# Kernel optimization log

Measured on AMD Instinct MI355X. Metric: run time of the kernel, lower is better.

## Reference

```python
import jax, jax.numpy as jnp
import numpy as np

S = 7
STEP = 1.0 / S
LAMBDA_COORD = 5.0
LAMBDA_NOOBJ = 0.5


def setup_inputs() -> dict:
    key = jax.random.key(0)
    k1, k2, k3 = jax.random.split(key, 3)
    B = 16384
    pred = jax.random.uniform(k1, (B, S, S, 30), dtype=jnp.float32)
    target = jax.random.uniform(k2, (B, S, S, 30), dtype=jnp.float32)
    conf = (jax.random.uniform(k3, (B, S, S)) > 0.9).astype(jnp.float32)
    target = target.at[..., 4].set(conf)
    return {"pred": pred, "target": target}


def _convert_box(box):
    # box: [..., S, S, 4] in cell-relative (x, y, w, h); returns clipped corners.
    gi = jnp.arange(S, dtype=box.dtype).reshape(1, S, 1)  # first spatial axis -> x offset
    gj = jnp.arange(S, dtype=box.dtype).reshape(1, 1, S)  # second spatial axis -> y offset
    x, y, w, h = box[..., 0], box[..., 1], box[..., 2], box[..., 3]
    cx = (x + gi) * STEP
    cy = (y + gj) * STEP
    x1 = jnp.maximum(cx - w / 2, 0.0)
    y1 = jnp.maximum(cy - h / 2, 0.0)
    x2 = jnp.minimum(cx + w / 2, 1.0)
    y2 = jnp.minimum(cy + h / 2, 1.0)
    return x1, y1, x2, y2


def _iou(b1, b2):
    a, b, c, d = b1
    q, w, e, r = b2
    minx = jnp.maximum(a, q)
    miny = jnp.maximum(b, w)
    maxx = jnp.minimum(c, e)
    maxy = jnp.minimum(d, r)
    inter = (maxy - miny) * (maxx - minx)  # faithful: no clamping of negative overlaps
    union = (e - q) * (r - w) + (d - b) * (c - a) - inter
    return jnp.where(inter > 0, inter / (union + 1e-05), 0.0)


def reference(pred, target):
    B = pred.shape[0]
    tbox = _convert_box(target[..., :4])
    pbox1 = _convert_box(pred[..., 0:4])
    pbox2 = _convert_box(pred[..., 5:9])
    iou1 = _iou(tbox, pbox1)  # [B, S, S]
    iou2 = _iou(tbox, pbox2)

    sel2 = iou1 <= iou2  # original: box1 responsible only if iou1 > iou2
    conf_t = jax.lax.stop_gradient(jnp.where(sel2, iou2, iou1))  # .item() detached iou
    pxy = jnp.where(sel2[..., None], pred[..., 5:7], pred[..., 0:2])
    pwh = jnp.where(sel2[..., None], pred[..., 7:9], pred[..., 2:4])
    pconf = jnp.where(sel2, pred[..., 9], pred[..., 4])

    obj = (target[..., 4] > 0).astype(pred.dtype)  # [B, S, S]
    noobj = (target[..., 4] == 0).astype(pred.dtype)

    obj_loss = jnp.sum(obj * (pconf - conf_t) ** 2)
    xy_loss = jnp.sum(obj[..., None] * (pxy - target[..., 0:2]) ** 2)
    wh_loss = jnp.sum(obj[..., None] * (pwh - target[..., 2:4]) ** 2)
    class_loss = jnp.sum(obj[..., None] * (pred[..., 10:] - target[..., 10:]) ** 2)
    noobj_loss = jnp.sum(noobj * ((pred[..., 4] - target[..., 4]) ** 2 + (pred[..., 9] - target[..., 9]) ** 2))

    loss = obj_loss + LAMBDA_NOOBJ * noobj_loss + LAMBDA_COORD * (xy_loss + wh_loss) + class_loss
    return loss / B
```

## Files before the change

### kernel.cpp

```cpp
#include <hip/hip_runtime.h>


#define NS 7
#define NC 30
#define CPB 128
#define BLOCK 128
#define CHUNK_FLOATS (CPB * NC)
#define GRID1 6272

typedef __attribute__((address_space(1))) const float global_float;
typedef __attribute__((address_space(3))) float lds_float;

__global__ __launch_bounds__(BLOCK) void yolo_loss_stage1(
    const float* __restrict__ pred,
    const float* __restrict__ targ,
    float* __restrict__ partials)
{
    const float STEP = 1.0f / 7.0f;
    const float L_COORD = 5.0f;
    const float L_NOOBJ = 0.5f;

    __shared__ float sbuf[2 * CHUNK_FLOATS];

    const int tid = threadIdx.x;
    const int wave = tid >> 6;
    const int lane = tid & 63;

    {
        const size_t base_bytes = (size_t)blockIdx.x * (CHUNK_FLOATS * 4);
        const char* gbase = (const char*)(wave == 0 ? pred : targ) + base_bytes
                          + (size_t)lane * 16;
        char* lbase = (char*)sbuf + wave * (CHUNK_FLOATS * 4);
        #pragma unroll
        for (int i = 0; i < 15; ++i) {
            __builtin_amdgcn_global_load_lds(
                (global_float*)(gbase + i * 1024),
                (lds_float*)(lbase + i * 1024),
                16, 0, 0);
        }
    }
    __syncthreads();

    const int cell = blockIdx.x * CPB + tid;
    const int j = cell % NS;
    const int i = (cell / NS) % NS;
    const float gi = (float)i;
    const float gj = (float)j;

    float p[NC], t[NC];
    {
        const float2* lp2 = (const float2*)(sbuf + tid * NC);
        const float2* lt2 = (const float2*)(sbuf + CHUNK_FLOATS + tid * NC);
        #pragma unroll
        for (int k = 0; k < NC / 2; ++k) {
            float2 v = lp2[k]; p[2 * k] = v.x; p[2 * k + 1] = v.y;
            float2 u = lt2[k]; t[2 * k] = u.x; t[2 * k + 1] = u.y;
        }
    }

    float ta, tb, tc, td;
    {
        float cx = (t[0] + gi) * STEP;
        float cy = (t[1] + gj) * STEP;
        ta = fmaxf(cx - t[2] * 0.5f, 0.0f);
        tb = fmaxf(cy - t[3] * 0.5f, 0.0f);
        tc = fminf(cx + t[2] * 0.5f, 1.0f);
        td = fminf(cy + t[3] * 0.5f, 1.0f);
    }
    float q1, w1, e1, r1;
    {
        float cx = (p[0] + gi) * STEP;
        float cy = (p[1] + gj) * STEP;
        q1 = fmaxf(cx - p[2] * 0.5f, 0.0f);
        w1 = fmaxf(cy - p[3] * 0.5f, 0.0f);
        e1 = fminf(cx + p[2] * 0.5f, 1.0f);
        r1 = fminf(cy + p[3] * 0.5f, 1.0f);
    }
    float q2, w2, e2, r2;
    {
        float cx = (p[5] + gi) * STEP;
        float cy = (p[6] + gj) * STEP;
        q2 = fmaxf(cx - p[7] * 0.5f, 0.0f);
        w2 = fmaxf(cy - p[8] * 0.5f, 0.0f);
        e2 = fminf(cx + p[7] * 0.5f, 1.0f);
        r2 = fminf(cy + p[8] * 0.5f, 1.0f);
    }

    float tarea = (td - tb) * (tc - ta);
    float iou1, iou2;
    {
        float minx = fmaxf(ta, q1), miny = fmaxf(tb, w1);
        float maxx = fminf(tc, e1), maxy = fminf(td, r1);
        float inter = (maxy - miny) * (maxx - minx);
        float uni = (e1 - q1) * (r1 - w1) + tarea - inter;
        iou1 = (inter > 0.0f) ? inter / (uni + 1e-5f) : 0.0f;
    }
    {
        float minx = fmaxf(ta, q2), miny = fmaxf(tb, w2);
        float maxx = fminf(tc, e2), maxy = fminf(td, r2);
        float inter = (maxy - miny) * (maxx - minx);
        float uni = (e2 - q2) * (r2 - w2) + tarea - inter;
        iou2 = (inter > 0.0f) ? inter / (uni + 1e-5f) : 0.0f;
    }

    bool sel2 = (iou1 <= iou2);
    float conf_t = sel2 ? iou2 : iou1;
    float px = sel2 ? p[5] : p[0];
    float py = sel2 ? p[6] : p[1];
    float pw = sel2 ? p[7] : p[2];
    float ph = sel2 ? p[8] : p[3];
    float pconf = sel2 ? p[9] : p[4];

    float obj = (t[4] > 0.0f) ? 1.0f : 0.0f;
    float noobj = (t[4] == 0.0f) ? 1.0f : 0.0f;

    float dx = px - t[0], dy = py - t[1];
    float dw = pw - t[2], dh = ph - t[3];
    float coord = dx * dx + dy * dy + dw * dw + dh * dh;

    float dc = pconf - conf_t;
    float obj_loss = dc * dc;

    float cls = 0.0f;
    #pragma unroll
    for (int k = 10; k < NC; ++k) {
        float d = p[k] - t[k];
        cls += d * d;
    }

    float d4 = p[4] - t[4];
    float d9 = p[9] - t[9];
    float noobj_loss = d4 * d4 + d9 * d9;

    float lsum = obj * (obj_loss + L_COORD * coord + cls) + L_NOOBJ * noobj * noobj_loss;

    #pragma unroll
    for (int off = 32; off > 0; off >>= 1)
        lsum += __shfl_down(lsum, off, 64);

    __shared__ float wsum[2];
    if (lane == 0) wsum[wave] = lsum;
    __syncthreads();
    if (tid == 0) {
        partials[blockIdx.x] = wsum[0] + wsum[1];
    }
}

__global__ __launch_bounds__(256) void yolo_loss_stage2(
    const float* __restrict__ partials, float* __restrict__ out, float inv_B)
{
    const int tid = threadIdx.x;
    float s = 0.0f;
    for (int k = tid; k < GRID1; k += 256)
        s += partials[k];

    #pragma unroll
    for (int off = 32; off > 0; off >>= 1)
        s += __shfl_down(s, off, 64);

    __shared__ float wsum[4];
    int lane = tid & 63;
    int wid = tid >> 6;
    if (lane == 0) wsum[wid] = s;
    __syncthreads();
    if (tid == 0)
        out[0] = (wsum[0] + wsum[1] + wsum[2] + wsum[3]) * inv_B;
}

extern "C" void kernel_launch(void* const* d_in, const int* in_sizes, int n_in,
                              void* d_out, int out_size, void* d_ws, size_t ws_size,
                              hipStream_t stream) {
    const float* pred = (const float*)d_in[0];
    const float* targ = (const float*)d_in[1];
    float* out = (float*)d_out;
    float* partials = (float*)d_ws;

    const float inv_B = 1.0f / 16384.0f;

    yolo_loss_stage1<<<GRID1, BLOCK, 0, stream>>>(pred, targ, partials);
    yolo_loss_stage2<<<1, 256, 0, stream>>>(partials, out, inv_B);
}
```

Measured before the change: 208.9 us.

## Replace LDS staging with direct float4 loads, two cells per thread

Drops the global_load_lds staging into shared memory and the barrier that followed it. Each thread now reads two adjacent cells (60 floats, 240 bytes) straight from global memory with float4 loads, and the block grows to 256 threads with a grid four times smaller. This removes the LDS round trip and synchronisation, but each lane's loads are strided by 240 bytes, so coalescing is worse and register use rises with 120 floats per thread.

```diff
diff --git a/kernel.cpp b/kernel.cpp
--- a/kernel.cpp
+++ b/kernel.cpp
@@ -3,105 +3,50 @@
 
 #define NS 7
 #define NC 30
-#define CPB 128
-#define BLOCK 128
-#define CHUNK_FLOATS (CPB * NC)
-#define GRID1 6272
+#define GRID1 1568
+#define BLOCK 256
 
-typedef __attribute__((address_space(1))) const float global_float;
-typedef __attribute__((address_space(3))) float lds_float;
-
-__global__ __launch_bounds__(BLOCK) void yolo_loss_stage1(
-    const float* __restrict__ pred,
-    const float* __restrict__ targ,
-    float* __restrict__ partials)
+__device__ __forceinline__ float cell_loss(const float* __restrict__ p,
+                                           const float* __restrict__ t,
+                                           float gi, float gj)
 {
     const float STEP = 1.0f / 7.0f;
     const float L_COORD = 5.0f;
     const float L_NOOBJ = 0.5f;
 
-    __shared__ float sbuf[2 * CHUNK_FLOATS];
+    float cx = (t[0] + gi) * STEP;
+    float cy = (t[1] + gj) * STEP;
+    float ta = fmaxf(cx - t[2] * 0.5f, 0.0f);
+    float tb = fmaxf(cy - t[3] * 0.5f, 0.0f);
+    float tc = fminf(cx + t[2] * 0.5f, 1.0f);
+    float td = fminf(cy + t[3] * 0.5f, 1.0f);
 
-    const int tid = threadIdx.x;
-    const int wave = tid >> 6;
-    const int lane = tid & 63;
+    cx = (p[0] + gi) * STEP;
+    cy = (p[1] + gj) * STEP;
+    float q1 = fmaxf(cx - p[2] * 0.5f, 0.0f);
+    float w1 = fmaxf(cy - p[3] * 0.5f, 0.0f);
+    float e1 = fminf(cx + p[2] * 0.5f, 1.0f);
+    float r1 = fminf(cy + p[3] * 0.5f, 1.0f);
 
-    {
-        const size_t base_bytes = (size_t)blockIdx.x * (CHUNK_FLOATS * 4);
-        const char* gbase = (const char*)(wave == 0 ? pred : targ) + base_bytes
-                          + (size_t)lane * 16;
-        char* lbase = (char*)sbuf + wave * (CHUNK_FLOATS * 4);
-        #pragma unroll
-        for (int i = 0; i < 15; ++i) {
-            __builtin_amdgcn_global_load_lds(
-                (global_float*)(gbase + i * 1024),
-                (lds_float*)(lbase + i * 1024),
-                16, 0, 0);
-        }
-    }
-    __syncthreads();
-
-    const int cell = blockIdx.x * CPB + tid;
-    const int j = cell % NS;
-    const int i = (cell / NS) % NS;
-    const float gi = (float)i;
-    const float gj = (float)j;
-
-    float p[NC], t[NC];
-    {
-        const float2* lp2 = (const float2*)(sbuf + tid * NC);
-        const float2* lt2 = (const float2*)(sbuf + CHUNK_FLOATS + tid * NC);
-        #pragma unroll
-        for (int k = 0; k < NC / 2; ++k) {
-            float2 v = lp2[k]; p[2 * k] = v.x; p[2 * k + 1] = v.y;
-            float2 u = lt2[k]; t[2 * k] = u.x; t[2 * k + 1] = u.y;
-        }
-    }
-
-    float ta, tb, tc, td;
-    {
-        float cx = (t[0] + gi) * STEP;
-        float cy = (t[1] + gj) * STEP;
-        ta = fmaxf(cx - t[2] * 0.5f, 0.0f);
-        tb = fmaxf(cy - t[3] * 0.5f, 0.0f);
-        tc = fminf(cx + t[2] * 0.5f, 1.0f);
-        td = fminf(cy + t[3] * 0.5f, 1.0f);
-    }
-    float q1, w1, e1, r1;
-    {
-        float cx = (p[0] + gi) * STEP;
-        float cy = (p[1] + gj) * STEP;
-        q1 = fmaxf(cx - p[2] * 0.5f, 0.0f);
-        w1 = fmaxf(cy - p[3] * 0.5f, 0.0f);
-        e1 = fminf(cx + p[2] * 0.5f, 1.0f);
-        r1 = fminf(cy + p[3] * 0.5f, 1.0f);
-    }
-    float q2, w2, e2, r2;
-    {
-        float cx = (p[5] + gi) * STEP;
-        float cy = (p[6] + gj) * STEP;
-        q2 = fmaxf(cx - p[7] * 0.5f, 0.0f);
-        w2 = fmaxf(cy - p[8] * 0.5f, 0.0f);
-        e2 = fminf(cx + p[7] * 0.5f, 1.0f);
-        r2 = fminf(cy + p[8] * 0.5f, 1.0f);
-    }
+    cx = (p[5] + gi) * STEP;
+    cy = (p[6] + gj) * STEP;
+    float q2 = fmaxf(cx - p[7] * 0.5f, 0.0f);
+    float w2 = fmaxf(cy - p[8] * 0.5f, 0.0f);
+    float e2 = fminf(cx + p[7] * 0.5f, 1.0f);
+    float r2 = fminf(cy + p[8] * 0.5f, 1.0f);
 
     float tarea = (td - tb) * (tc - ta);
-    float iou1, iou2;
-    {
-        float minx = fmaxf(ta, q1), miny = fmaxf(tb, w1);
-        float maxx = fminf(tc, e1), maxy = fminf(td, r1);
-        float inter = (maxy - miny) * (maxx - minx);
-        float uni = (e1 - q1) * (r1 - w1) + tarea - inter;
-        iou1 = (inter > 0.0f) ? inter / (uni + 1e-5f) : 0.0f;
-    }
-    {
-        float minx = fmaxf(ta, q2), miny = fmaxf(tb, w2);
-        float maxx = fminf(tc, e2), maxy = fminf(td, r2);
-        float inter = (maxy - miny) * (maxx - minx);
-        float uni = (e2 - q2) * (r2 - w2) + tarea - inter;
-        iou2 = (inter > 0.0f) ? inter / (uni + 1e-5f) : 0.0f;
-    }
+    float minx = fmaxf(ta, q1), miny = fmaxf(tb, w1);
+    float maxx = fminf(tc, e1), maxy = fminf(td, r1);
+    float inter = (maxy - miny) * (maxx - minx);
+    float uni = (e1 - q1) * (r1 - w1) + tarea - inter;
+    float iou1 = (inter > 0.0f) ? inter / (uni + 1e-5f) : 0.0f;
+
+    minx = fmaxf(ta, q2); miny = fmaxf(tb, w2);
+    maxx = fminf(tc, e2); maxy = fminf(td, r2);
+    inter = (maxy - miny) * (maxx - minx);
+    uni = (e2 - q2) * (r2 - w2) + tarea - inter;
+    float iou2 = (inter > 0.0f) ? inter / (uni + 1e-5f) : 0.0f;
 
     bool sel2 = (iou1 <= iou2);
     float conf_t = sel2 ? iou2 : iou1;
@@ -132,18 +77,53 @@
     float d9 = p[9] - t[9];
     float noobj_loss = d4 * d4 + d9 * d9;
 
-    float lsum = obj * (obj_loss + L_COORD * coord + cls) + L_NOOBJ * noobj * noobj_loss;
+    return obj * (obj_loss + L_COORD * coord + cls) + L_NOOBJ * noobj * noobj_loss;
+}
+
+__global__ __launch_bounds__(BLOCK) void yolo_loss_stage1(
+    const float* __restrict__ pred,
+    const float* __restrict__ targ,
+    float* __restrict__ partials)
+{
+    const int tid = threadIdx.x;
+    const int task = blockIdx.x * BLOCK + tid;
+    const int cell0 = task * 2;
+
+    const float4* __restrict__ gp4 = (const float4*)pred + (size_t)task * 15;
+    const float4* __restrict__ gt4 = (const float4*)targ + (size_t)task * 15;
+
+    float p[2 * NC], t[2 * NC];
+    #pragma unroll
+    for (int k = 0; k < 15; ++k) {
+        float4 v = gp4[k];
+        p[4 * k + 0] = v.x; p[4 * k + 1] = v.y; p[4 * k + 2] = v.z; p[4 * k + 3] = v.w;
+    }
+    #pragma unroll
+    for (int k = 0; k < 15; ++k) {
+        float4 u = gt4[k];
+        t[4 * k + 0] = u.x; t[4 * k + 1] = u.y; t[4 * k + 2] = u.z; t[4 * k + 3] = u.w;
+    }
+
+    int j0 = cell0 % NS;
+    int i0 = (cell0 / NS) % NS;
+    int c1 = cell0 + 1;
+    int j1 = c1 % NS;
+    int i1 = (c1 / NS) % NS;
+
+    float lsum = cell_loss(p, t, (float)i0, (float)j0)
+               + cell_loss(p + NC, t + NC, (float)i1, (float)j1);
 
     #pragma unroll
     for (int off = 32; off > 0; off >>= 1)
         lsum += __shfl_down(lsum, off, 64);
 
-    __shared__ float wsum[2];
-    if (lane == 0) wsum[wave] = lsum;
+    __shared__ float wsum[4];
+    int lane = tid & 63;
+    int wid = tid >> 6;
+    if (lane == 0) wsum[wid] = lsum;
     __syncthreads();
-    if (tid == 0) {
-        partials[blockIdx.x] = wsum[0] + wsum[1];
-    }
+    if (tid == 0)
+        partials[blockIdx.x] = (wsum[0] + wsum[1]) + (wsum[2] + wsum[3]);
 }
 
 __global__ __launch_bounds__(256) void yolo_loss_stage2(
```

After: 211.0 us. No clear change (+1.0%).
